# Kernel tuning notes

Measured on AMD Instinct MI355X. Metric: run time of the kernel, lower is better.

## Reference

```python
import jax, jax.numpy as jnp
import numpy as np

B, C_IN, H, W = 2, 256, 48, 48
OC, G, KH, KW, PH, PW = 256, 4, 7, 7, 3, 3


def _patches(y, Hn, Wn):
    # y: (B, C, Hp, Wp) -> (B, C, KH, KW, Hn, Wn); stride=1, dilation=1
    return jnp.stack([
        jnp.stack([y[:, :, i:i + Hn, j:j + Wn] for j in range(KW)], axis=2)
        for i in range(KH)
    ], axis=2)


def setup_inputs() -> dict:
    key = jax.random.key(0)
    k1, k2, k3, k4 = jax.random.split(key, 4)
    fan_out = 3 * OC  # 1x1 conv, kaiming fan_out
    conv_w = jax.random.normal(k2, (3 * OC, C_IN), dtype=jnp.float32) * np.sqrt(2.0 / fan_out).astype(np.float32)
    return {
        "x": jax.random.normal(k1, (B, C_IN, H, W), dtype=jnp.float32),
        "conv_w": conv_w,
        "rpe_h": jax.random.normal(k3, (G, 1, KH, 1, (OC // G) // 2), dtype=jnp.float32),
        "rpe_w": jax.random.normal(k4, (G, 1, 1, KW, (OC // G) // 2), dtype=jnp.float32),
    }


def reference(x, conv_w, rpe_h, rpe_w):
    b, c, h, w = x.shape
    goc = OC // G
    c2 = goc // 2
    K = KH * KW
    center = (K - 1) // 2
    ci, cj = center // KW, center % KW

    # 1x1 conv to 3*OC channels, then zero-pad (equiv. to Conv2d(padding) + bias=False)
    y = jnp.einsum('bchw,oc->bohw', x, conv_w)
    y = jnp.pad(y, ((0, 0), (0, 0), (PH, PH), (PW, PW)))
    Hn = h + 2 * PH - (KH - 1)
    Wn = w + 2 * PW - (KW - 1)
    P = Hn * Wn

    q_full, k_full, v_full = jnp.split(y, 3, axis=1)

    # query: only the center element of each window is used
    query = q_full[:, :, ci:ci + Hn, cj:cj + Wn].reshape(b, G, goc, P)
    query = jnp.transpose(query, (0, 1, 3, 2))  # (B,G,P,goc)

    # key: full windows + relative position embeddings
    kp = _patches(k_full, Hn, Wn).reshape(b, G, goc, KH, KW, P)
    key = jnp.transpose(kp, (0, 1, 5, 3, 4, 2))  # (B,G,P,KH,KW,goc)
    key = jnp.concatenate((key[..., :c2] + rpe_h, key[..., c2:] + rpe_w), axis=1)  # (B,2G,P,KH,KW,c2)
    key = key.reshape(b, G, P, K, goc)  # row-major reshape matches torch

    vp = _patches(v_full, Hn, Wn).reshape(b, G, goc, K, P)
    value = jnp.transpose(vp, (0, 1, 4, 3, 2))  # (B,G,P,K,goc)

    att = jax.nn.softmax(jnp.einsum('bgpc,bgpkc->bgpk', query, key), axis=-1)
    out = jnp.einsum('bgpk,bgpkc->bgpc', att, value)  # (B,G,P,goc)
    out = jnp.transpose(out, (0, 1, 3, 2)).reshape(b, OC, Hn, Wn)
    return out
```

## Files before the change

### kernel.cpp

```cpp
#include <hip/hip_runtime.h>

#define BB   2
#define CIN  256
#define OC3  768
#define NG   4
#define GOC  64
#define C2   32
#define KK   49
#define PP   2304
#define HALF_P 1152

#define RS      56
#define BROWS   54
#define BSTRIDE (BROWS * RS * OC3)
#define IOFF    ((3 * RS + 3) * OC3)

#define Y2_BYTES  (BB * BROWS * RS * OC3 * 4)
#define XT_OFF    Y2_BYTES
#define WT_OFF    (XT_OFF + BB * PP * 512 * 2)

typedef __attribute__((ext_vector_type(8))) short bf16x8;
typedef __attribute__((ext_vector_type(4))) float f32x4;

static __device__ __forceinline__ unsigned short f2bf_rne(float x) {
    unsigned int u = __float_as_uint(x);
    unsigned int r = u + 0x7FFFu + ((u >> 16) & 1u);
    return (unsigned short)(r >> 16);
}
static __device__ __forceinline__ float bf2f(unsigned short h) {
    return __uint_as_float(((unsigned int)h) << 16);
}

static __device__ __forceinline__ void gll16(const short* g, short* l) {
    __builtin_amdgcn_global_load_lds(
        (const __attribute__((address_space(1))) unsigned int*)g,
        (__attribute__((address_space(3))) unsigned int*)l,
        16, 0, 0);
}

template <int C>
static __device__ __forceinline__ float dppf(float x) {
    return __int_as_float(__builtin_amdgcn_update_dpp(
        0, __float_as_int(x), C, 0xF, 0xF, true));
}
template <int D>
static __device__ __forceinline__ float xor_lane(float x) {
    if constexpr (D == 1)       return dppf<0xB1>(x);
    else if constexpr (D == 2)  return dppf<0x4E>(x);
    else if constexpr (D == 4)  return dppf<0x141>(dppf<0x4E>(dppf<0xB1>(x)));
    else if constexpr (D == 8)  return dppf<0x128>(x);
    else                        return __shfl_xor(x, D, 64);
}
template <int N> struct IC { static constexpr int value = N; };

#define ROW4  (RS * OC3 / 4)
#define REG1  (6 * ROW4)
#define COLS4 (OC3 / 4)

__global__ __launch_bounds__(256) void prep(
    const float* __restrict__ W, short* __restrict__ Wt,
    const float* __restrict__ X, short* __restrict__ Xt)
{
    __shared__ float tile[64][65];
    const int bid = blockIdx.x;
    const int t   = threadIdx.x;

    if (bid < 768) {
        int tt = bid * 256 + t;
        int o = tt >> 8, c = tt & 255;
        float v = W[tt];
        unsigned short hi = f2bf_rne(v);
        unsigned short lo = f2bf_rne(v - bf2f(hi));
        Wt[(size_t)o * 512 + c]       = (short)hi;
        Wt[(size_t)o * 512 + 256 + c] = (short)lo;
    } else {
        const int blk = bid - 768;
        const int p0  = (blk % 36) * 64;
        const int c0  = ((blk / 36) & 3) * 64;
        const int b   = blk / 144;

        const float* Xb = X + (size_t)b * CIN * PP;
        #pragma unroll
        for (int r = 0; r < 16; ++r) {
            int idx = r * 256 + t;
            int c = idx >> 6, p = idx & 63;
            tile[c][p] = Xb[(size_t)(c0 + c) * PP + p0 + p];
        }
        __syncthreads();
        short* Xo = Xt + (size_t)b * PP * 512;
        #pragma unroll
        for (int r = 0; r < 16; ++r) {
            int idx = r * 256 + t;
            int p = idx >> 6, c = idx & 63;
            float v = tile[c][p];
            unsigned short hi = f2bf_rne(v);
            unsigned short lo = f2bf_rne(v - bf2f(hi));
            size_t base = (size_t)(p0 + p) * 512 + c0 + c;
            Xo[base]       = (short)hi;
            Xo[base + 256] = (short)lo;
        }
    }
}

__global__ __launch_bounds__(256, 4) void conv_mfma(
    const short* __restrict__ Wt,
    const short* __restrict__ Xt,
    float* __restrict__ Y2)
{
    __shared__ short As[2][64 * 32];
    __shared__ short Bs[2][64 * 32];

    const int tid = threadIdx.x;
    const int bn  = blockIdx.x;
    const int bm  = blockIdx.y;
    const int b   = blockIdx.z;

    if (bm >= 12) {
        const int idx = ((bm - 12) * 36 + bn) * 256 + tid;
        float4* Yb = (float4*)(Y2 + (size_t)b * BSTRIDE);
        const float4 z = make_float4(0.f, 0.f, 0.f, 0.f);
        if (idx < REG1) {
            int r6  = idx / ROW4;
            int rem = idx - r6 * ROW4;
            int r   = (r6 < 3) ? r6 : 48 + r6;
            Yb[r * ROW4 + rem] = z;
        } else {
            int i2  = idx - REG1;
            int r   = 3 + i2 / (8 * COLS4);
            int rem = i2 - (r - 3) * (8 * COLS4);
            int cg  = rem / COLS4;
            int c   = (cg < 3) ? cg : 48 + cg;
            int ch4 = rem - cg * COLS4;
            Yb[(r * RS + c) * COLS4 + ch4] = z;
        }
        return;
    }

    const int om0 = bm * 64, pn0 = bn * 64;

    const int lane = tid & 63, w = tid >> 6;
    const int oq = (w & 1) * 32, pq = (w >> 1) * 32;
    const int ln15 = lane & 15, q = lane >> 4;

    const int R  = (w << 4) + (lane >> 2);
    const int sd = (lane & 3) ^ ((R >> 1) & 3);
    const short* gAq = Wt + (size_t)(om0 + R) * 512 + sd * 8;
    const short* gBq = Xt + (size_t)b * PP * 512 + (size_t)(pn0 + R) * 512 + sd * 8;

    const int swz = q ^ ((ln15 >> 1) & 3);

    f32x4 acc[2][2] = {};

    gll16(gAq + 0, &As[0][w * 512]);
    gll16(gBq + 0, &Bs[0][w * 512]);
    __syncthreads();

    for (int t = 0; t < 24; ++t) {
        const int cur = t & 1;

        bf16x8 af[2], bf[2];
        #pragma unroll
        for (int i = 0; i < 2; ++i) {
            af[i] = *(const bf16x8*)&As[cur][(oq + i * 16 + ln15) * 32 + swz * 8];
            bf[i] = *(const bf16x8*)&Bs[cur][(pq + i * 16 + ln15) * 32 + swz * 8];
        }

        if (t < 23) {
            const int k0 = 32 * (t + 1);
            const int wk = (k0 < 256) ? k0 : k0 - 256;
            const int xk = (k0 < 512) ? k0 : k0 - 512;
            gll16(gAq + wk, &As[cur ^ 1][w * 512]);
            gll16(gBq + xk, &Bs[cur ^ 1][w * 512]);
        }

        #pragma unroll
        for (int i = 0; i < 2; ++i)
            #pragma unroll
            for (int j = 0; j < 2; ++j)
                acc[i][j] = __builtin_amdgcn_mfma_f32_16x16x32_bf16(
                    af[i], bf[j], acc[i][j], 0, 0, 0);

        if (t < 23) __syncthreads();
    }

    float* Yb = Y2 + (size_t)b * BSTRIDE + IOFF;
    #pragma unroll
    for (int i = 0; i < 2; ++i) {
        #pragma unroll
        for (int j = 0; j < 2; ++j) {
            int o = om0 + oq + i * 16 + q * 4;
            int p = pn0 + pq + j * 16 + ln15;
            int h = p / 48, ww = p - h * 48;
            *(f32x4*)&Yb[(size_t)(h * RS + ww) * OC3 + o] = acc[i][j];
        }
    }
}

struct TagH { static constexpr bool value = true;  };
struct TagW { static constexpr bool value = false; };

__global__ __launch_bounds__(256, 6) void attn_kernel(
    const float* __restrict__ Y2,
    const float* __restrict__ rpe_h,
    const float* __restrict__ rpe_w,
    float* __restrict__ out)
{
    __shared__ float xpose[4][65];

    const int tid  = threadIdx.x;
    const int lane = tid & 63;
    const int w    = tid >> 6;
    const int bx     = blockIdx.x;
    const int wblock = (bx & 7) * 576 + (bx >> 3);
    const int wid    = wblock * 4 + w;
    const int pq   = wid % PP;
    const int g    = (wid / PP) & (NG - 1);
    const int b    = wid / (PP * NG);
    const int ph   = pq / 48;
    const int pw   = pq - ph * 48;

    const float* Yb = Y2 + (size_t)b * BSTRIDE + IOFF;

    const float qv = Yb[(size_t)(ph * RS + pw) * OC3 + g * GOC + lane];

    const int t   = (pq >= HALF_P) ? 1 : 0;
    const int qpr = pq - t * HALF_P;
    const int p0  = 2 * qpr;
    const int ph0 = p0 / 48;
    const int pw0 = p0 - ph0 * 48;
    const int g2  = 2 * g + t;
    const bool use_h = (g2 < NG);
    const int  kch   = use_h ? (CIN + g2 * GOC) : (CIN + (g2 - NG) * GOC + C2);
    const float* rb  = use_h ? (rpe_h + g2 * 7 * C2) : (rpe_w + (g2 - NG) * 7 * C2);

    const int  c  = lane & 31;
    const bool hi = (lane >= 32);

    const float R0 = rb[0 * C2 + c], R1 = rb[1 * C2 + c], R2 = rb[2 * C2 + c],
                R3 = rb[3 * C2 + c], R4 = rb[4 * C2 + c], R5 = rb[5 * C2 + c],
                R6 = rb[6 * C2 + c];

    const float* kb = Yb + (size_t)(ph0 * RS + pw0) * OC3 + kch + c;

    auto rget = [&](int idx) -> float {
        return idx == 0 ? R0 : idx == 1 ? R1 : idx == 2 ? R2 :
               idx == 3 ? R3 : idx == 4 ? R4 : idx == 5 ? R5 : R6;
    };

    auto tree = [&](auto tag) -> float {
        constexpr bool UH = decltype(tag)::value;
        auto chunkprod = [&](int l) -> float {
            int m0 = 2 * l,     h10 = (m0 >= KK), k0 = m0 - KK * h10;
            int m1 = 2 * l + 1, h11 = (m1 >= KK), k1 = m1 - KK * h11;
            int i0 = k0 / 7, j0 = k0 % 7, i1 = k1 / 7, j1 = k1 % 7;
            int d0 = ((i0 - 3) * RS + (h10 + j0 - 3)) * OC3;
            int d1 = ((i1 - 3) * RS + (h11 + j1 - 3)) * OC3;
            float kv = kb[hi ? d1 : d0];
            float ra = UH ? rget(i0) : rget(j0);
            float rc = UH ? rget(i1) : rget(j1);
            kv += hi ? rc : ra;
            return qv * kv;
        };
        auto val = [&](int jj) -> float {
            if (2 * jj >= KK) return 0.f;
            float pa = chunkprod(2 * jj);
            float pb = (2 * jj + 1 < KK) ? chunkprod(2 * jj + 1) : 0.f;
            float u  = (lane & 1) ? pb : pa;
            float ww = (lane & 1) ? pa : pb;
            return u + xor_lane<1>(ww);
        };
        auto comb = [&](auto dc, float x, float y) -> float {
            constexpr int d = decltype(dc)::value;
            float u  = (lane & d) ? y : x;
            float ww = (lane & d) ? x : y;
            return u + xor_lane<d>(ww);
        };
        float acc32[2];
        #pragma unroll
        for (int a = 0; a < 2; ++a) {
            float acc16[2];
            #pragma unroll
            for (int bq = 0; bq < 2; ++bq) {
                float acc8[2];
                #pragma unroll
                for (int cq2 = 0; cq2 < 2; ++cq2) {
                    float acc4t[2];
                    #pragma unroll
                    for (int dq = 0; dq < 2; ++dq) {
                        float acc2[2];
                        #pragma unroll
                        for (int eq = 0; eq < 2; ++eq)
                            acc2[eq] = val(a * 16 + bq * 8 + cq2 * 4 + dq * 2 + eq);
                        acc4t[dq] = comb(IC<2>{}, acc2[0], acc2[1]);
                    }
                    acc8[cq2] = comb(IC<4>{}, acc4t[0], acc4t[1]);
                }
                acc16[bq] = comb(IC<8>{}, acc8[0], acc8[1]);
            }
            acc32[a] = comb(IC<16>{}, acc16[0], acc16[1]);
        }
        return comb(IC<32>{}, acc32[0], acc32[1]);
    };

    const float logit = use_h ? tree(TagH{}) : tree(TagW{});

    float mx = logit;
    mx = fmaxf(mx, xor_lane<1>(mx));
    mx = fmaxf(mx, xor_lane<2>(mx));
    mx = fmaxf(mx, xor_lane<4>(mx));
    mx = fmaxf(mx, xor_lane<8>(mx));
    mx = fmaxf(mx, xor_lane<16>(mx));
    mx = fmaxf(mx, xor_lane<32>(mx));
    float e = (lane < KK) ? __expf(logit - mx) : 0.f;
    float ssum = e;
    ssum += xor_lane<1>(ssum);
    ssum += xor_lane<2>(ssum);
    ssum += xor_lane<4>(ssum);
    ssum += xor_lane<8>(ssum);
    ssum += xor_lane<16>(ssum);
    ssum += xor_lane<32>(ssum);
    const float att = e / ssum;

    float acc = 0.f;
    const float* vb = Yb + (size_t)(ph * RS + pw) * OC3 + 2 * CIN + g * GOC + lane;
    #pragma unroll
    for (int k = 0; k < KK; ++k) {
        int i = k / 7, j = k % 7;
        int doff = ((i - 3) * RS + (j - 3)) * OC3;
        float ak = __uint_as_float(
            __builtin_amdgcn_readlane(__float_as_uint(att), k));
        acc = fmaf(ak, vb[doff], acc);
    }

    xpose[w][lane] = acc;
    __syncthreads();
    const int wid0 = wblock * 4;
    const int pq0  = wid0 % PP;
    const int g0   = (wid0 / PP) & (NG - 1);
    const int b0   = wid0 / (PP * NG);
    const int ch   = tid >> 2;
    const int w2   = tid & 3;
    out[((size_t)b0 * 256 + g0 * GOC + ch) * PP + pq0 + w2] = xpose[w2][ch];
}

extern "C" void kernel_launch(void* const* d_in, const int* in_sizes, int n_in,
                              void* d_out, int out_size, void* d_ws, size_t ws_size,
                              hipStream_t stream)
{
    const float* x  = (const float*)d_in[0];
    const float* w  = (const float*)d_in[1];
    const float* rh = (const float*)d_in[2];
    const float* rw = (const float*)d_in[3];

    float* Y2 = (float*)d_ws;
    short* Xt = (short*)((char*)d_ws + XT_OFF);
    short* Wt = (short*)((char*)d_ws + WT_OFF);

    prep<<<1056, 256, 0, stream>>>(w, Wt, x, Xt);
    conv_mfma<<<dim3(36, 27, BB), 256, 0, stream>>>(Wt, Xt, Y2);
    attn_kernel<<<(BB * NG * PP) / 4, 256, 0, stream>>>(Y2, rh, rw, (float*)d_out);
}
```

Measured before the change: 109.4 us.

## Store key and value projections as bf16 in separate compact padded buffers

The conv kernel now writes the K and V projections as bf16 into two separate 256-channel padded buffers, while Q stays fp32 in the original layout. The attention kernel gathers K and V from these compact buffers, which halves the bytes per element and shrinks the row stride. The aim is to cut memory traffic and improve cache locality in the gather-heavy attention kernel. Only K and V halos are zeroed now, so the zero-fill grid shrinks. The cost is reduced precision in keys and values, which could affect accuracy against the fp32 reference.

```diff
diff --git a/kernel.cpp b/kernel.cpp
--- a/kernel.cpp
+++ b/kernel.cpp
@@ -15,12 +15,18 @@
 #define BSTRIDE (BROWS * RS * OC3)
 #define IOFF    ((3 * RS + 3) * OC3)
 
+#define BS2    (BROWS * RS * 256)
+#define IOFF2  ((3 * RS + 3) * 256)
+
 #define Y2_BYTES  (BB * BROWS * RS * OC3 * 4)
 #define XT_OFF    Y2_BYTES
 #define WT_OFF    (XT_OFF + BB * PP * 512 * 2)
+#define K2_OFF    (WT_OFF + 768 * 512 * 2)
+#define V2_OFF    (K2_OFF + BB * BS2 * 2)
 
 typedef __attribute__((ext_vector_type(8))) short bf16x8;
 typedef __attribute__((ext_vector_type(4))) float f32x4;
+typedef __attribute__((ext_vector_type(4))) unsigned short u16x4;
 
 static __device__ __forceinline__ unsigned short f2bf_rne(float x) {
     unsigned int u = __float_as_uint(x);
@@ -52,10 +58,6 @@
     else                        return __shfl_xor(x, D, 64);
 }
 template <int N> struct IC { static constexpr int value = N; };
-
-#define ROW4  (RS * OC3 / 4)
-#define REG1  (6 * ROW4)
-#define COLS4 (OC3 / 4)
 
 __global__ __launch_bounds__(256) void prep(
     const float* __restrict__ W, short* __restrict__ Wt,
@@ -105,7 +107,9 @@
 __global__ __launch_bounds__(256, 4) void conv_mfma(
     const short* __restrict__ Wt,
     const short* __restrict__ Xt,
-    float* __restrict__ Y2)
+    float* __restrict__ Y2,
+    unsigned short* __restrict__ K2,
+    unsigned short* __restrict__ V2)
 {
     __shared__ short As[2][64 * 32];
     __shared__ short Bs[2][64 * 32];
@@ -117,22 +121,21 @@
 
     if (bm >= 12) {
         const int idx = ((bm - 12) * 36 + bn) * 256 + tid;
-        float4* Yb = (float4*)(Y2 + (size_t)b * BSTRIDE);
-        const float4 z = make_float4(0.f, 0.f, 0.f, 0.f);
-        if (idx < REG1) {
-            int r6  = idx / ROW4;
-            int rem = idx - r6 * ROW4;
-            int r   = (r6 < 3) ? r6 : 48 + r6;
-            Yb[r * ROW4 + rem] = z;
+        const int half = 23040;
+        unsigned short* buf = ((idx < half) ? K2 : V2) + (size_t)b * BS2;
+        const int id2  = (idx < half) ? idx : idx - half;
+        const int cell = id2 >> 5;
+        const int chnk = id2 & 31;
+        int r, ccol;
+        if (cell < 336) {
+            int r6 = cell / 56; ccol = cell - r6 * 56;
+            r = (r6 < 3) ? r6 : 48 + r6;
         } else {
-            int i2  = idx - REG1;
-            int r   = 3 + i2 / (8 * COLS4);
-            int rem = i2 - (r - 3) * (8 * COLS4);
-            int cg  = rem / COLS4;
-            int c   = (cg < 3) ? cg : 48 + cg;
-            int ch4 = rem - cg * COLS4;
-            Yb[(r * RS + c) * COLS4 + ch4] = z;
-        }
+            int i2 = cell - 336; r = 3 + (i2 >> 3);
+            int cg = i2 & 7; ccol = (cg < 3) ? cg : 48 + cg;
+        }
+        uint4* p = (uint4*)(buf + (size_t)(r * RS + ccol) * 256) + chnk;
+        *p = make_uint4(0u, 0u, 0u, 0u);
         return;
     }
 
@@ -183,15 +186,33 @@
         if (t < 23) __syncthreads();
     }
 
-    float* Yb = Y2 + (size_t)b * BSTRIDE + IOFF;
-    #pragma unroll
-    for (int i = 0; i < 2; ++i) {
-        #pragma unroll
-        for (int j = 0; j < 2; ++j) {
-            int o = om0 + oq + i * 16 + q * 4;
-            int p = pn0 + pq + j * 16 + ln15;
-            int h = p / 48, ww = p - h * 48;
-            *(f32x4*)&Yb[(size_t)(h * RS + ww) * OC3 + o] = acc[i][j];
+    if (bm < 4) {
+        float* Yb = Y2 + (size_t)b * BSTRIDE + IOFF;
+        #pragma unroll
+        for (int i = 0; i < 2; ++i) {
+            #pragma unroll
+            for (int j = 0; j < 2; ++j) {
+                int o = om0 + oq + i * 16 + q * 4;
+                int p = pn0 + pq + j * 16 + ln15;
+                int h = p / 48, ww = p - h * 48;
+                *(f32x4*)&Yb[(size_t)(h * RS + ww) * OC3 + o] = acc[i][j];
+            }
+        }
+    } else {
+        unsigned short* dst = ((bm < 8) ? K2 : V2) + (size_t)b * BS2 + IOFF2;
+        const int obase = om0 - ((bm < 8) ? 256 : 512);
+        #pragma unroll
+        for (int i = 0; i < 2; ++i) {
+            #pragma unroll
+            for (int j = 0; j < 2; ++j) {
+                int o = obase + oq + i * 16 + q * 4;
+                int p = pn0 + pq + j * 16 + ln15;
+                int h = p / 48, ww = p - h * 48;
+                u16x4 pk;
+                #pragma unroll
+                for (int cc = 0; cc < 4; ++cc) pk[cc] = f2bf_rne(acc[i][j][cc]);
+                *(u16x4*)&dst[(size_t)(h * RS + ww) * 256 + o] = pk;
+            }
         }
     }
 }
@@ -201,6 +222,8 @@
 
 __global__ __launch_bounds__(256, 6) void attn_kernel(
     const float* __restrict__ Y2,
+    const unsigned short* __restrict__ K2,
+    const unsigned short* __restrict__ V2,
     const float* __restrict__ rpe_h,
     const float* __restrict__ rpe_w,
     float* __restrict__ out)
@@ -230,7 +253,7 @@
     const int pw0 = p0 - ph0 * 48;
     const int g2  = 2 * g + t;
     const bool use_h = (g2 < NG);
-    const int  kch   = use_h ? (CIN + g2 * GOC) : (CIN + (g2 - NG) * GOC + C2);
+    const int  kch2  = use_h ? (g2 * GOC) : ((g2 - NG) * GOC + C2);
     const float* rb  = use_h ? (rpe_h + g2 * 7 * C2) : (rpe_w + (g2 - NG) * 7 * C2);
 
     const int  c  = lane & 31;
@@ -240,7 +263,8 @@
                 R3 = rb[3 * C2 + c], R4 = rb[4 * C2 + c], R5 = rb[5 * C2 + c],
                 R6 = rb[6 * C2 + c];
 
-    const float* kb = Yb + (size_t)(ph0 * RS + pw0) * OC3 + kch + c;
+    const unsigned short* kb = K2 + (size_t)b * BS2 + IOFF2
+                             + (size_t)(ph0 * RS + pw0) * 256 + kch2 + c;
 
     auto rget = [&](int idx) -> float {
         return idx == 0 ? R0 : idx == 1 ? R1 : idx == 2 ? R2 :
@@ -253,9 +277,9 @@
             int m0 = 2 * l,     h10 = (m0 >= KK), k0 = m0 - KK * h10;
             int m1 = 2 * l + 1, h11 = (m1 >= KK), k1 = m1 - KK * h11;
             int i0 = k0 / 7, j0 = k0 % 7, i1 = k1 / 7, j1 = k1 % 7;
-            int d0 = ((i0 - 3) * RS + (h10 + j0 - 3)) * OC3;
-            int d1 = ((i1 - 3) * RS + (h11 + j1 - 3)) * OC3;
-            float kv = kb[hi ? d1 : d0];
+            int d0 = ((i0 - 3) * RS + (h10 + j0 - 3)) * 256;
+            int d1 = ((i1 - 3) * RS + (h11 + j1 - 3)) * 256;
+            float kv = bf2f(kb[hi ? d1 : d0]);
             float ra = UH ? rget(i0) : rget(j0);
             float rc = UH ? rget(i1) : rget(j1);
             kv += hi ? rc : ra;
@@ -322,14 +346,15 @@
     const float att = e / ssum;
 
     float acc = 0.f;
-    const float* vb = Yb + (size_t)(ph * RS + pw) * OC3 + 2 * CIN + g * GOC + lane;
+    const unsigned short* vb = V2 + (size_t)b * BS2 + IOFF2
+                             + (size_t)(ph * RS + pw) * 256 + g * GOC + lane;
     #pragma unroll
     for (int k = 0; k < KK; ++k) {
         int i = k / 7, j = k % 7;
-        int doff = ((i - 3) * RS + (j - 3)) * OC3;
+        int doff = ((i - 3) * RS + (j - 3)) * 256;
         float ak = __uint_as_float(
             __builtin_amdgcn_readlane(__float_as_uint(att), k));
-        acc = fmaf(ak, vb[doff], acc);
+        acc = fmaf(ak, bf2f(vb[doff]), acc);
     }
 
     xpose[w][lane] = acc;
@@ -355,8 +380,10 @@
     float* Y2 = (float*)d_ws;
     short* Xt = (short*)((char*)d_ws + XT_OFF);
     short* Wt = (short*)((char*)d_ws + WT_OFF);
+    unsigned short* K2 = (unsigned short*)((char*)d_ws + K2_OFF);
+    unsigned short* V2 = (unsigned short*)((char*)d_ws + V2_OFF);
 
     prep<<<1056, 256, 0, stream>>>(w, Wt, x, Xt);
-    conv_mfma<<<dim3(36, 27, BB), 256, 0, stream>>>(Wt, Xt, Y2);
-    attn_kernel<<<(BB * NG * PP) / 4, 256, 0, stream>>>(Y2, rh, rw, (float*)d_out);
-}
+    conv_mfma<<<dim3(36, 17, BB), 256, 0, stream>>>(Wt, Xt, Y2, K2, V2);
+    attn_kernel<<<(BB * NG * PP) / 4, 256, 0, stream>>>(Y2, K2, V2, rh, rw, (float*)d_out);
+}
```

Result: faster. 103.8 us, median of 2 (-5.1%).
